# Performance work log

Measured on AMD Instinct MI355X. Metric: run time of the kernel, lower is better.

## Reference

```python
import jax, jax.numpy as jnp
import numpy as np
from math import sqrt

T_TEMP = 1.0  # softmax temperature (init arg T)
NEG_INF = -1e30  # finite stand-in for -inf; masked probs are exactly 0 after softmax


def setup_inputs() -> dict:
    key = jax.random.key(0)
    kq, kk, kv = jax.random.split(key, 3)
    B, L, H, E = 4, 2048, 16, 64
    queries = jax.random.normal(kq, (B, L, H, E), dtype=jnp.float32)
    keys = jax.random.normal(kk, (B, L, H, E), dtype=jnp.float32)
    values = jax.random.normal(kv, (B, L, H, E), dtype=jnp.float32)
    return {"queries": queries, "keys": keys, "values": values}


def reference(queries, keys, values):
    # queries: [B,L,H,E], keys: [B,S,H,E], values: [B,S,H,D]
    B, L, H, E = queries.shape
    S = keys.shape[1]
    scale = 1.0 / sqrt(E)
    # scores: [B,H,L,S]
    scores = jnp.einsum('blhe,bshe->bhls', queries, keys) * scale
    # causal mask: True above diagonal -> masked out (TriangularCausalMask)
    causal = jnp.triu(jnp.ones((L, S), dtype=bool), k=1)
    scores = jnp.where(causal, NEG_INF, scores)
    A = jax.nn.softmax(scores / T_TEMP, axis=-1)  # dropout p=0 -> identity
    V = jnp.einsum('bhls,bshd->blhd', A, values)
    return V
```

## Files before the change

### kernel.cpp

```cpp
#include <hip/hip_runtime.h>


typedef __attribute__((ext_vector_type(8))) unsigned short u16x8;
typedef __attribute__((ext_vector_type(4))) unsigned short u16x4;
typedef __attribute__((ext_vector_type(8))) __bf16 bf16x8;
typedef __attribute__((ext_vector_type(4))) float f32x4;

#define LOG2E 1.44269504088896340736f
#define AS1 __attribute__((address_space(1)))
#define AS3 __attribute__((address_space(3)))

static __device__ __forceinline__ unsigned short f32_bf16_rne(float x) {
    unsigned int b = __builtin_bit_cast(unsigned int, x);
    b = (b + 0x7fffu + ((b >> 16) & 1u)) >> 16;
    return (unsigned short)b;
}

static __device__ __forceinline__ int swzs(int row) {
    return (row & 6) | ((row >> 3) & 1);
}
static __device__ __forceinline__ int tileIdx(int row, int col) {
    return row * 64 + (((col >> 3) ^ swzs(row)) << 3) + (col & 7);
}

__global__ __launch_bounds__(256) void prep_kernel(
    const float* __restrict__ K, const float* __restrict__ V,
    unsigned short* __restrict__ wsK, unsigned short* __restrict__ wsV)
{
    const int ROW = 1024;
    const int tid = threadIdx.x;
    const int kt  = blockIdx.x;
    const int bh  = blockIdx.y;
    const size_t tileBase = (size_t)(bh >> 4) * 2048 * ROW + (size_t)(bh & 15) * 64
                          + (size_t)(kt * 64) * ROW;
    unsigned short* kimg = wsK + (((size_t)bh * 32 + kt) << 12);
    unsigned short* vimg = wsV + (((size_t)bh * 32 + kt) << 12);

    const int kRow = tid >> 4, kCol = (tid & 15) * 4;
    #pragma unroll
    for (int j = 0; j < 4; ++j) {
        const int key = j * 16 + kRow;
        f32x4 v = *(const f32x4*)(K + tileBase + (size_t)key * ROW + kCol);
        u16x4 w;
        #pragma unroll
        for (int i = 0; i < 4; ++i) w[i] = f32_bf16_rne(v[i]);
        *(u16x4*)&kimg[tileIdx(key, kCol)] = w;
    }
    const int vKey2 = (tid & 31) * 2, vDbase = (tid >> 5) * 8;
    const float* r0 = V + tileBase + (size_t)vKey2 * ROW + vDbase;
    #pragma unroll
    for (int j = 0; j < 2; ++j) {
        f32x4 va = *(const f32x4*)(r0 + j * 4);
        f32x4 vb = *(const f32x4*)(r0 + ROW + j * 4);
        #pragma unroll
        for (int i = 0; i < 4; ++i) {
            unsigned int pk = (unsigned int)f32_bf16_rne(va[i])
                            | ((unsigned int)f32_bf16_rne(vb[i]) << 16);
            *(unsigned int*)&vimg[tileIdx(vDbase + j * 4 + i, vKey2)] = pk;
        }
    }
}

__global__ __launch_bounds__(256, 4) void fattn2_kernel(
    const float* __restrict__ Q,
    const unsigned short* __restrict__ wsK,
    const unsigned short* __restrict__ wsV,
    float* __restrict__ O)
{
    const int ROW = 1024;

    const int tid  = threadIdx.x;
    const int wave = tid >> 6;
    const int lane = tid & 63;
    const int quad = lane >> 4;
    const int n16  = lane & 15;

    const int id   = blockIdx.x;
    const int k8   = id & 7;
    const int rest = id >> 3;
    const int bh   = k8 * 8 + (rest >> 4);
    const int xb   = rest & 15;
    const size_t headBase = (size_t)(bh >> 4) * 2048 * ROW + (size_t)(bh & 15) * 64;

    __shared__ __align__(16) unsigned short sK[2][4096];
    __shared__ __align__(16) unsigned short sV[2][4096];
    __shared__ __align__(16) unsigned short sP[4][1024];

    int kvIdx[4];
    #pragma unroll
    for (int nb = 0; nb < 4; ++nb) {
        const int row = nb * 16 + n16;
        kvIdx[nb] = row * 64 + ((quad ^ swzs(row)) << 3);
    }
    const int pIdx = n16 * 64 + ((quad ^ swzs(n16)) << 3);

    const float c0 = 0.125f * LOG2E;

    for (int qi = 0; qi < 2; ++qi) {
        const int qtile = qi ? (31 - xb) : xb;
        const int q0 = qtile * 64 + wave * 16;

        bf16x8 qf0, qf1;
        {
            const float* qrow = Q + headBase + (size_t)(q0 + n16) * ROW + quad * 8;
            u16x8 a, b;
            #pragma unroll
            for (int i = 0; i < 8; ++i) {
                a[i] = f32_bf16_rne(qrow[i] * c0);
                b[i] = f32_bf16_rne(qrow[32 + i] * c0);
            }
            qf0 = __builtin_bit_cast(bf16x8, a);
            qf1 = __builtin_bit_cast(bf16x8, b);
        }

        f32x4 oacc[4];
        #pragma unroll
        for (int d = 0; d < 4; ++d) oacc[d] = (f32x4){0.f, 0.f, 0.f, 0.f};
        float l_r[4];
        #pragma unroll
        for (int r = 0; r < 4; ++r) l_r[r] = 0.f;

        const int nT = qtile + 1;

        #define STAGE(buf, kt_)                                                   \
        do {                                                                      \
            const size_t toff = (((size_t)bh * 32 + (kt_)) << 12);                \
            const unsigned short* kg = wsK + toff + wave * 1024 + lane * 8;       \
            const unsigned short* vg = wsV + toff + wave * 1024 + lane * 8;       \
            __builtin_amdgcn_global_load_lds((const AS1 unsigned int*)kg,         \
                (AS3 unsigned int*)&sK[buf][wave * 1024], 16, 0, 0);              \
            __builtin_amdgcn_global_load_lds((const AS1 unsigned int*)(kg + 512), \
                (AS3 unsigned int*)&sK[buf][wave * 1024 + 512], 16, 0, 0);        \
            __builtin_amdgcn_global_load_lds((const AS1 unsigned int*)vg,         \
                (AS3 unsigned int*)&sV[buf][wave * 1024], 16, 0, 0);              \
            __builtin_amdgcn_global_load_lds((const AS1 unsigned int*)(vg + 512), \
                (AS3 unsigned int*)&sV[buf][wave * 1024 + 512], 16, 0, 0);        \
        } while (0)

        __syncthreads();
        STAGE(0, 0);

        for (int kt = 0; kt < nT; ++kt) {
            const int cur = kt & 1;

            __syncthreads();

            if (kt + 1 < nT) STAGE(cur ^ 1, kt + 1);

            f32x4 sacc[4];
            #pragma unroll
            for (int nb = 0; nb < 4; ++nb) {
                bf16x8 b0 = __builtin_bit_cast(bf16x8, *(const u16x8*)&sK[cur][kvIdx[nb]]);
                bf16x8 b1 = __builtin_bit_cast(bf16x8, *(const u16x8*)&sK[cur][kvIdx[nb] ^ 32]);
                f32x4 s = (f32x4){0.f, 0.f, 0.f, 0.f};
                s = __builtin_amdgcn_mfma_f32_16x16x32_bf16(qf0, b0, s, 0, 0, 0);
                s = __builtin_amdgcn_mfma_f32_16x16x32_bf16(qf1, b1, s, 0, 0, 0);
                sacc[nb] = s;
            }

            if (kt == qtile) {
                #pragma unroll
                for (int nb = 0; nb < 4; ++nb) {
                    const int keyl = nb * 16 + n16;
                    #pragma unroll
                    for (int r = 0; r < 4; ++r) {
                        const int ql = wave * 16 + quad * 4 + r;
                        sacc[nb][r] = (keyl > ql) ? -1e30f : sacc[nb][r];
                    }
                }
            }

            #pragma unroll
            for (int r = 0; r < 4; ++r) {
                const int qrl = quad * 4 + r;
                const int pwBase = qrl * 64 + (n16 & 7);
                const int sw = swzs(qrl);
                const int hb = n16 >> 3;
                float ps = 0.f;
                #pragma unroll
                for (int nb = 0; nb < 4; ++nb) {
                    unsigned short u = f32_bf16_rne(__builtin_amdgcn_exp2f(sacc[nb][r]));
                    ps += __builtin_bit_cast(float, (unsigned int)u << 16);
                    sP[wave][pwBase + (((nb * 2 + hb) ^ sw) << 3)] = u;
                }
                l_r[r] += ps;
            }

            #pragma unroll
            for (int kh = 0; kh < 2; ++kh) {
                bf16x8 ap = __builtin_bit_cast(bf16x8,
                    *(const u16x8*)&sP[wave][pIdx ^ (kh << 5)]);
                #pragma unroll
                for (int d = 0; d < 4; ++d) {
                    bf16x8 vf = __builtin_bit_cast(bf16x8,
                        *(const u16x8*)&sV[cur][kvIdx[d] ^ (kh << 5)]);
                    oacc[d] = __builtin_amdgcn_mfma_f32_16x16x32_bf16(ap, vf, oacc[d], 0, 0, 0);
                }
            }
        }
        #undef STAGE

        float inv[4];
        #pragma unroll
        for (int r = 0; r < 4; ++r) {
            float l = l_r[r];
            #pragma unroll
            for (int off = 1; off < 16; off <<= 1)
                l += __shfl_xor(l, off, 64);
            inv[r] = 1.0f / l;
        }
        #pragma unroll
        for (int d = 0; d < 4; ++d) {
            #pragma unroll
            for (int r = 0; r < 4; ++r) {
                const int qg = q0 + quad * 4 + r;
                O[headBase + (size_t)qg * ROW + d * 16 + n16] = oacc[d][r] * inv[r];
            }
        }
    }
}

__global__ __launch_bounds__(256, 4) void fattn_kernel(
    const float* __restrict__ Q,
    const float* __restrict__ K,
    const float* __restrict__ V,
    float* __restrict__ O)
{
    const int ROW = 1024;
    const int tid  = threadIdx.x;
    const int wave = tid >> 6;
    const int lane = tid & 63;
    const int quad = lane >> 4;
    const int n16  = lane & 15;
    const int xb = blockIdx.x;
    const int bh = blockIdx.y;
    const size_t headBase = (size_t)(bh >> 4) * 2048 * ROW + (size_t)(bh & 15) * 64;

    __shared__ __align__(16) unsigned short sK[4096];
    __shared__ __align__(16) unsigned short sV[4096];
    __shared__ __align__(16) unsigned short sP[4][1024];

    int kvIdx[4];
    #pragma unroll
    for (int nb = 0; nb < 4; ++nb) {
        const int row = nb * 16 + n16;
        kvIdx[nb] = row * 64 + ((quad ^ swzs(row)) << 3);
    }
    const int pIdx = n16 * 64 + ((quad ^ swzs(n16)) << 3);
    const int kStageRow = tid >> 4;
    const int kStageCol = (tid & 15) * 4;
    const int vKey2  = (tid & 31) * 2;
    const int vDbase = (tid >> 5) * 8;
    const float c0 = 0.125f * LOG2E;

    for (int qi = 0; qi < 2; ++qi) {
        const int qtile = qi ? (31 - xb) : xb;
        const int q0 = qtile * 64 + wave * 16;
        bf16x8 qf0, qf1;
        {
            const float* qrow = Q + headBase + (size_t)(q0 + n16) * ROW + quad * 8;
            u16x8 a, b;
            #pragma unroll
            for (int i = 0; i < 8; ++i) {
                a[i] = f32_bf16_rne(qrow[i] * c0);
                b[i] = f32_bf16_rne(qrow[32 + i] * c0);
            }
            qf0 = __builtin_bit_cast(bf16x8, a);
            qf1 = __builtin_bit_cast(bf16x8, b);
        }
        f32x4 oacc[4];
        #pragma unroll
        for (int d = 0; d < 4; ++d) oacc[d] = (f32x4){0.f, 0.f, 0.f, 0.f};
        float l_r[4];
        #pragma unroll
        for (int r = 0; r < 4; ++r) l_r[r] = 0.f;
        const int nT = qtile + 1;
        f32x4 pk[4], pva[2], pvb[2];
        {
            const float* kb = K + headBase;
            const float* r0 = V + headBase + (size_t)vKey2 * ROW + vDbase;
            #pragma unroll
            for (int j = 0; j < 4; ++j)
                pk[j] = *(const f32x4*)(kb + (size_t)(j * 16 + kStageRow) * ROW + kStageCol);
            #pragma unroll
            for (int j = 0; j < 2; ++j) {
                pva[j] = *(const f32x4*)(r0 + j * 4);
                pvb[j] = *(const f32x4*)(r0 + ROW + j * 4);
            }
        }
        for (int kt = 0; kt < nT; ++kt) {
            __syncthreads();
            #pragma unroll
            for (int j = 0; j < 4; ++j) {
                u16x4 w;
                #pragma unroll
                for (int i = 0; i < 4; ++i) w[i] = f32_bf16_rne(pk[j][i]);
                *(u16x4*)&sK[tileIdx(j * 16 + kStageRow, kStageCol)] = w;
            }
            #pragma unroll
            for (int j = 0; j < 2; ++j) {
                const int d0 = vDbase + j * 4;
                #pragma unroll
                for (int i = 0; i < 4; ++i) {
                    unsigned int pkk = (unsigned int)f32_bf16_rne(pva[j][i])
                                     | ((unsigned int)f32_bf16_rne(pvb[j][i]) << 16);
                    *(unsigned int*)&sV[tileIdx(d0 + i, vKey2)] = pkk;
                }
            }
            if (kt + 1 < nT) {
                const size_t nb2 = headBase + (size_t)((kt + 1) * 64) * ROW;
                const float* kb = K + nb2;
                const float* r0 = V + nb2 + (size_t)vKey2 * ROW + vDbase;
                #pragma unroll
                for (int j = 0; j < 4; ++j)
                    pk[j] = *(const f32x4*)(kb + (size_t)(j * 16 + kStageRow) * ROW + kStageCol);
                #pragma unroll
                for (int j = 0; j < 2; ++j) {
                    pva[j] = *(const f32x4*)(r0 + j * 4);
                    pvb[j] = *(const f32x4*)(r0 + ROW + j * 4);
                }
            }
            __syncthreads();
            f32x4 sacc[4];
            #pragma unroll
            for (int nb = 0; nb < 4; ++nb) {
                bf16x8 b0 = __builtin_bit_cast(bf16x8, *(const u16x8*)&sK[kvIdx[nb]]);
                bf16x8 b1 = __builtin_bit_cast(bf16x8, *(const u16x8*)&sK[kvIdx[nb] ^ 32]);
                f32x4 s = (f32x4){0.f, 0.f, 0.f, 0.f};
                s = __builtin_amdgcn_mfma_f32_16x16x32_bf16(qf0, b0, s, 0, 0, 0);
                s = __builtin_amdgcn_mfma_f32_16x16x32_bf16(qf1, b1, s, 0, 0, 0);
                sacc[nb] = s;
            }
            if (kt == qtile) {
                #pragma unroll
                for (int nb = 0; nb < 4; ++nb) {
                    const int keyl = nb * 16 + n16;
                    #pragma unroll
                    for (int r = 0; r < 4; ++r) {
                        const int ql = wave * 16 + quad * 4 + r;
                        sacc[nb][r] = (keyl > ql) ? -1e30f : sacc[nb][r];
                    }
                }
            }
            #pragma unroll
            for (int r = 0; r < 4; ++r) {
                const int qrl = quad * 4 + r;
                const int pwBase = qrl * 64 + (n16 & 7);
                const int sw = swzs(qrl);
                const int hb = n16 >> 3;
                float ps = 0.f;
                #pragma unroll
                for (int nb = 0; nb < 4; ++nb) {
                    unsigned short u = f32_bf16_rne(__builtin_amdgcn_exp2f(sacc[nb][r]));
                    ps += __builtin_bit_cast(float, (unsigned int)u << 16);
                    sP[wave][pwBase + (((nb * 2 + hb) ^ sw) << 3)] = u;
                }
                l_r[r] += ps;
            }
            #pragma unroll
            for (int kh = 0; kh < 2; ++kh) {
                bf16x8 ap = __builtin_bit_cast(bf16x8,
                    *(const u16x8*)&sP[wave][pIdx ^ (kh << 5)]);
                #pragma unroll
                for (int d = 0; d < 4; ++d) {
                    bf16x8 vf = __builtin_bit_cast(bf16x8,
                        *(const u16x8*)&sV[kvIdx[d] ^ (kh << 5)]);
                    oacc[d] = __builtin_amdgcn_mfma_f32_16x16x32_bf16(ap, vf, oacc[d], 0, 0, 0);
                }
            }
        }
        float inv[4];
        #pragma unroll
        for (int r = 0; r < 4; ++r) {
            float l = l_r[r];
            #pragma unroll
            for (int off = 1; off < 16; off <<= 1)
                l += __shfl_xor(l, off, 64);
            inv[r] = 1.0f / l;
        }
        #pragma unroll
        for (int d = 0; d < 4; ++d) {
            #pragma unroll
            for (int r = 0; r < 4; ++r) {
                const int qg = q0 + quad * 4 + r;
                O[headBase + (size_t)qg * ROW + d * 16 + n16] = oacc[d][r] * inv[r];
            }
        }
    }
}

extern "C" void kernel_launch(void* const* d_in, const int* in_sizes, int n_in,
                              void* d_out, int out_size, void* d_ws, size_t ws_size,
                              hipStream_t stream) {
    const float* Q = (const float*)d_in[0];
    const float* K = (const float*)d_in[1];
    const float* V = (const float*)d_in[2];
    float* Out = (float*)d_out;

    const size_t imgElems = (size_t)64 * 32 * 4096;
    if (ws_size >= imgElems * 2 * sizeof(unsigned short)) {
        unsigned short* wsK = (unsigned short*)d_ws;
        unsigned short* wsV = wsK + imgElems;
        hipLaunchKernelGGL(prep_kernel, dim3(32, 64), dim3(256), 0, stream, K, V, wsK, wsV);
        hipLaunchKernelGGL(fattn2_kernel, dim3(1024), dim3(256), 0, stream, Q, wsK, wsV, Out);
    } else {
        hipLaunchKernelGGL(fattn_kernel, dim3(16, 64), dim3(256), 0, stream, Q, K, V, Out);
    }
}
```

Baseline: 200.1 us.

## Keep softmax probabilities in registers, transpose MFMA, one q-tile per block

The attention kernel now computes S^T by swapping MFMA operands, so each lane holds probabilities for a single query row. P is rearranged into B-operand layout with cross-lane shuffles instead of a round trip through shared memory, which removes the sP buffer. Each block now handles one q-tile, longest first, over 2048 blocks with launch bounds raised to 5 blocks per CU. Output is transposed through LDS for coalesced f32x4 stores, and conversions use packed v_cvt_pk_bf16_f32. The prep kernel transposes V through padded LDS so global writes are vectorized. The cost is extra shuffles, register pressure from the higher occupancy target, and less even load balance across blocks.

```diff
diff --git a/kernel.cpp b/kernel.cpp
--- a/kernel.cpp
+++ b/kernel.cpp
@@ -5,6 +5,7 @@
 typedef __attribute__((ext_vector_type(4))) unsigned short u16x4;
 typedef __attribute__((ext_vector_type(8))) __bf16 bf16x8;
 typedef __attribute__((ext_vector_type(4))) float f32x4;
+typedef __attribute__((ext_vector_type(4))) unsigned int u32x4;
 
 #define LOG2E 1.44269504088896340736f
 #define AS1 __attribute__((address_space(1)))
@@ -14,6 +15,12 @@
     unsigned int b = __builtin_bit_cast(unsigned int, x);
     b = (b + 0x7fffu + ((b >> 16) & 1u)) >> 16;
     return (unsigned short)b;
+}
+
+static __device__ __forceinline__ unsigned int cvt_pk_bf16(float lo, float hi) {
+    unsigned int r;
+    asm("v_cvt_pk_bf16_f32 %0, %1, %2" : "=v"(r) : "v"(lo), "v"(hi));
+    return r;
 }
 
 static __device__ __forceinline__ int swzs(int row) {
@@ -36,6 +43,8 @@
     unsigned short* kimg = wsK + (((size_t)bh * 32 + kt) << 12);
     unsigned short* vimg = wsV + (((size_t)bh * 32 + kt) << 12);
 
+    __shared__ unsigned int sT[64 * 33];
+
     const int kRow = tid >> 4, kCol = (tid & 15) * 4;
     #pragma unroll
     for (int j = 0; j < 4; ++j) {
@@ -46,22 +55,33 @@
         for (int i = 0; i < 4; ++i) w[i] = f32_bf16_rne(v[i]);
         *(u16x4*)&kimg[tileIdx(key, kCol)] = w;
     }
-    const int vKey2 = (tid & 31) * 2, vDbase = (tid >> 5) * 8;
-    const float* r0 = V + tileBase + (size_t)vKey2 * ROW + vDbase;
-    #pragma unroll
-    for (int j = 0; j < 2; ++j) {
-        f32x4 va = *(const f32x4*)(r0 + j * 4);
-        f32x4 vb = *(const f32x4*)(r0 + ROW + j * 4);
-        #pragma unroll
-        for (int i = 0; i < 4; ++i) {
-            unsigned int pk = (unsigned int)f32_bf16_rne(va[i])
-                            | ((unsigned int)f32_bf16_rne(vb[i]) << 16);
-            *(unsigned int*)&vimg[tileIdx(vDbase + j * 4 + i, vKey2)] = pk;
-        }
-    }
-}
-
-__global__ __launch_bounds__(256, 4) void fattn2_kernel(
+
+    const int rp = tid >> 3;
+    const int cc = tid & 7;
+    const float* v0 = V + tileBase + (size_t)(2 * rp) * ROW + cc * 8;
+    f32x4 a0 = *(const f32x4*)(v0);
+    f32x4 a1 = *(const f32x4*)(v0 + 4);
+    f32x4 b0 = *(const f32x4*)(v0 + ROW);
+    f32x4 b1 = *(const f32x4*)(v0 + ROW + 4);
+    #pragma unroll
+    for (int i = 0; i < 4; ++i) {
+        sT[(cc * 8 + i) * 33 + rp]     = cvt_pk_bf16(a0[i], b0[i]);
+        sT[(cc * 8 + 4 + i) * 33 + rp] = cvt_pk_bf16(a1[i], b1[i]);
+    }
+    __syncthreads();
+    const int d = tid >> 2;
+    #pragma unroll
+    for (int it = 0; it < 2; ++it) {
+        const int p = (tid & 3) + it * 4;
+        const int c = p ^ swzs(d);
+        u32x4 w;
+        #pragma unroll
+        for (int j = 0; j < 4; ++j) w[j] = sT[d * 33 + c * 4 + j];
+        *(u32x4*)&vimg[(size_t)d * 64 + p * 8] = w;
+    }
+}
+
+__global__ __launch_bounds__(256, 5) void fattn2_kernel(
     const float* __restrict__ Q,
     const unsigned short* __restrict__ wsK,
     const unsigned short* __restrict__ wsV,
@@ -74,17 +94,19 @@
     const int lane = tid & 63;
     const int quad = lane >> 4;
     const int n16  = lane & 15;
-
-    const int id   = blockIdx.x;
-    const int k8   = id & 7;
-    const int rest = id >> 3;
-    const int bh   = k8 * 8 + (rest >> 4);
-    const int xb   = rest & 15;
+    const bool hi16 = (lane & 16) != 0;
+    const bool hi32 = (lane & 32) != 0;
+
+    const int id    = blockIdx.x;
+    const int k8    = id & 7;
+    const int rest  = id >> 3;
+    const int bh    = k8 * 8 + (rest >> 5);
+    const int qtile = 31 - (rest & 31);
     const size_t headBase = (size_t)(bh >> 4) * 2048 * ROW + (size_t)(bh & 15) * 64;
+    const int q0 = qtile * 64 + wave * 16;
 
     __shared__ __align__(16) unsigned short sK[2][4096];
     __shared__ __align__(16) unsigned short sV[2][4096];
-    __shared__ __align__(16) unsigned short sP[4][1024];
 
     int kvIdx[4];
     #pragma unroll
@@ -92,131 +114,153 @@
         const int row = nb * 16 + n16;
         kvIdx[nb] = row * 64 + ((quad ^ swzs(row)) << 3);
     }
-    const int pIdx = n16 * 64 + ((quad ^ swzs(n16)) << 3);
 
     const float c0 = 0.125f * LOG2E;
 
-    for (int qi = 0; qi < 2; ++qi) {
-        const int qtile = qi ? (31 - xb) : xb;
-        const int q0 = qtile * 64 + wave * 16;
-
-        bf16x8 qf0, qf1;
-        {
-            const float* qrow = Q + headBase + (size_t)(q0 + n16) * ROW + quad * 8;
-            u16x8 a, b;
-            #pragma unroll
-            for (int i = 0; i < 8; ++i) {
-                a[i] = f32_bf16_rne(qrow[i] * c0);
-                b[i] = f32_bf16_rne(qrow[32 + i] * c0);
-            }
-            qf0 = __builtin_bit_cast(bf16x8, a);
-            qf1 = __builtin_bit_cast(bf16x8, b);
-        }
-
-        f32x4 oacc[4];
-        #pragma unroll
-        for (int d = 0; d < 4; ++d) oacc[d] = (f32x4){0.f, 0.f, 0.f, 0.f};
-        float l_r[4];
-        #pragma unroll
-        for (int r = 0; r < 4; ++r) l_r[r] = 0.f;
-
-        const int nT = qtile + 1;
-
-        #define STAGE(buf, kt_)                                                   \
-        do {                                                                      \
-            const size_t toff = (((size_t)bh * 32 + (kt_)) << 12);                \
-            const unsigned short* kg = wsK + toff + wave * 1024 + lane * 8;       \
-            const unsigned short* vg = wsV + toff + wave * 1024 + lane * 8;       \
-            __builtin_amdgcn_global_load_lds((const AS1 unsigned int*)kg,         \
-                (AS3 unsigned int*)&sK[buf][wave * 1024], 16, 0, 0);              \
-            __builtin_amdgcn_global_load_lds((const AS1 unsigned int*)(kg + 512), \
-                (AS3 unsigned int*)&sK[buf][wave * 1024 + 512], 16, 0, 0);        \
-            __builtin_amdgcn_global_load_lds((const AS1 unsigned int*)vg,         \
-                (AS3 unsigned int*)&sV[buf][wave * 1024], 16, 0, 0);              \
-            __builtin_amdgcn_global_load_lds((const AS1 unsigned int*)(vg + 512), \
-                (AS3 unsigned int*)&sV[buf][wave * 1024 + 512], 16, 0, 0);        \
-        } while (0)
+    bf16x8 qf0, qf1;
+    {
+        const float* qrow = Q + headBase + (size_t)(q0 + n16) * ROW + quad * 8;
+        f32x4 qv0 = *(const f32x4*)(qrow);
+        f32x4 qv1 = *(const f32x4*)(qrow + 4);
+        f32x4 qv2 = *(const f32x4*)(qrow + 32);
+        f32x4 qv3 = *(const f32x4*)(qrow + 36);
+        u32x4 a, b;
+        a[0] = cvt_pk_bf16(qv0[0] * c0, qv0[1] * c0);
+        a[1] = cvt_pk_bf16(qv0[2] * c0, qv0[3] * c0);
+        a[2] = cvt_pk_bf16(qv1[0] * c0, qv1[1] * c0);
+        a[3] = cvt_pk_bf16(qv1[2] * c0, qv1[3] * c0);
+        b[0] = cvt_pk_bf16(qv2[0] * c0, qv2[1] * c0);
+        b[1] = cvt_pk_bf16(qv2[2] * c0, qv2[3] * c0);
+        b[2] = cvt_pk_bf16(qv3[0] * c0, qv3[1] * c0);
+        b[3] = cvt_pk_bf16(qv3[2] * c0, qv3[3] * c0);
+        qf0 = __builtin_bit_cast(bf16x8, a);
+        qf1 = __builtin_bit_cast(bf16x8, b);
+    }
+
+    f32x4 oacc[4];
+    #pragma unroll
+    for (int dd = 0; dd < 4; ++dd) oacc[dd] = (f32x4){0.f, 0.f, 0.f, 0.f};
+    float l = 0.f;
+
+    const int nT = qtile + 1;
+
+    #define STAGE(buf, kt_)                                                   \
+    do {                                                                      \
+        const size_t toff = (((size_t)bh * 32 + (kt_)) << 12);                \
+        const unsigned short* kg = wsK + toff + wave * 1024 + lane * 8;       \
+        const unsigned short* vg = wsV + toff + wave * 1024 + lane * 8;       \
+        __builtin_amdgcn_global_load_lds((const AS1 unsigned int*)kg,         \
+            (AS3 unsigned int*)&sK[buf][wave * 1024], 16, 0, 0);              \
+        __builtin_amdgcn_global_load_lds((const AS1 unsigned int*)(kg + 512), \
+            (AS3 unsigned int*)&sK[buf][wave * 1024 + 512], 16, 0, 0);        \
+        __builtin_amdgcn_global_load_lds((const AS1 unsigned int*)vg,         \
+            (AS3 unsigned int*)&sV[buf][wave * 1024], 16, 0, 0);              \
+        __builtin_amdgcn_global_load_lds((const AS1 unsigned int*)(vg + 512), \
+            (AS3 unsigned int*)&sV[buf][wave * 1024 + 512], 16, 0, 0);        \
+    } while (0)
+
+    STAGE(0, 0);
+
+    for (int kt = 0; kt < nT; ++kt) {
+        const int cur = kt & 1;
 
         __syncthreads();
-        STAGE(0, 0);
-
-        for (int kt = 0; kt < nT; ++kt) {
-            const int cur = kt & 1;
-
-            __syncthreads();
-
-            if (kt + 1 < nT) STAGE(cur ^ 1, kt + 1);
-
-            f32x4 sacc[4];
+
+        if (kt + 1 < nT) STAGE(cur ^ 1, kt + 1);
+
+        f32x4 sacc[4];
+        #pragma unroll
+        for (int nb = 0; nb < 4; ++nb) {
+            bf16x8 b0 = __builtin_bit_cast(bf16x8, *(const u16x8*)&sK[cur][kvIdx[nb]]);
+            bf16x8 b1 = __builtin_bit_cast(bf16x8, *(const u16x8*)&sK[cur][kvIdx[nb] ^ 32]);
+            f32x4 s = (f32x4){0.f, 0.f, 0.f, 0.f};
+            s = __builtin_amdgcn_mfma_f32_16x16x32_bf16(b0, qf0, s, 0, 0, 0);
+            s = __builtin_amdgcn_mfma_f32_16x16x32_bf16(b1, qf1, s, 0, 0, 0);
+            sacc[nb] = s;
+        }
+
+        if (kt == qtile) {
+            const int ql = wave * 16 + n16;
             #pragma unroll
             for (int nb = 0; nb < 4; ++nb) {
-                bf16x8 b0 = __builtin_bit_cast(bf16x8, *(const u16x8*)&sK[cur][kvIdx[nb]]);
-                bf16x8 b1 = __builtin_bit_cast(bf16x8, *(const u16x8*)&sK[cur][kvIdx[nb] ^ 32]);
-                f32x4 s = (f32x4){0.f, 0.f, 0.f, 0.f};
-                s = __builtin_amdgcn_mfma_f32_16x16x32_bf16(qf0, b0, s, 0, 0, 0);
-                s = __builtin_amdgcn_mfma_f32_16x16x32_bf16(qf1, b1, s, 0, 0, 0);
-                sacc[nb] = s;
-            }
-
-            if (kt == qtile) {
-                #pragma unroll
-                for (int nb = 0; nb < 4; ++nb) {
-                    const int keyl = nb * 16 + n16;
-                    #pragma unroll
-                    for (int r = 0; r < 4; ++r) {
-                        const int ql = wave * 16 + quad * 4 + r;
-                        sacc[nb][r] = (keyl > ql) ? -1e30f : sacc[nb][r];
-                    }
-                }
-            }
-
-            #pragma unroll
-            for (int r = 0; r < 4; ++r) {
-                const int qrl = quad * 4 + r;
-                const int pwBase = qrl * 64 + (n16 & 7);
-                const int sw = swzs(qrl);
-                const int hb = n16 >> 3;
-                float ps = 0.f;
-                #pragma unroll
-                for (int nb = 0; nb < 4; ++nb) {
-                    unsigned short u = f32_bf16_rne(__builtin_amdgcn_exp2f(sacc[nb][r]));
-                    ps += __builtin_bit_cast(float, (unsigned int)u << 16);
-                    sP[wave][pwBase + (((nb * 2 + hb) ^ sw) << 3)] = u;
-                }
-                l_r[r] += ps;
-            }
-
-            #pragma unroll
-            for (int kh = 0; kh < 2; ++kh) {
-                bf16x8 ap = __builtin_bit_cast(bf16x8,
-                    *(const u16x8*)&sP[wave][pIdx ^ (kh << 5)]);
-                #pragma unroll
-                for (int d = 0; d < 4; ++d) {
-                    bf16x8 vf = __builtin_bit_cast(bf16x8,
-                        *(const u16x8*)&sV[cur][kvIdx[d] ^ (kh << 5)]);
-                    oacc[d] = __builtin_amdgcn_mfma_f32_16x16x32_bf16(ap, vf, oacc[d], 0, 0, 0);
-                }
-            }
-        }
-        #undef STAGE
-
-        float inv[4];
-        #pragma unroll
-        for (int r = 0; r < 4; ++r) {
-            float l = l_r[r];
-            #pragma unroll
-            for (int off = 1; off < 16; off <<= 1)
-                l += __shfl_xor(l, off, 64);
-            inv[r] = 1.0f / l;
-        }
-        #pragma unroll
-        for (int d = 0; d < 4; ++d) {
-            #pragma unroll
-            for (int r = 0; r < 4; ++r) {
-                const int qg = q0 + quad * 4 + r;
-                O[headBase + (size_t)qg * ROW + d * 16 + n16] = oacc[d][r] * inv[r];
-            }
-        }
+                #pragma unroll
+                for (int r = 0; r < 4; ++r) {
+                    const int keyl = nb * 16 + quad * 4 + r;
+                    sacc[nb][r] = (keyl > ql) ? -1e30f : sacc[nb][r];
+                }
+            }
+        }
+
+        unsigned int W[4][2];
+        float psum = 0.f;
+        #pragma unroll
+        for (int nb = 0; nb < 4; ++nb) {
+            float p0 = __builtin_amdgcn_exp2f(sacc[nb][0]);
+            float p1 = __builtin_amdgcn_exp2f(sacc[nb][1]);
+            float p2 = __builtin_amdgcn_exp2f(sacc[nb][2]);
+            float p3 = __builtin_amdgcn_exp2f(sacc[nb][3]);
+            psum += (p0 + p1) + (p2 + p3);
+            W[nb][0] = cvt_pk_bf16(p0, p1);
+            W[nb][1] = cvt_pk_bf16(p2, p3);
+        }
+        l += psum;
+
+        #pragma unroll
+        for (int kh = 0; kh < 2; ++kh) {
+            const unsigned int A0 = W[2 * kh][0],     A1 = W[2 * kh][1];
+            const unsigned int B0 = W[2 * kh + 1][0], B1 = W[2 * kh + 1][1];
+            const unsigned int sA0 = __shfl_xor(A0, 32, 64);
+            const unsigned int sB0 = __shfl_xor(B0, 32, 64);
+            const unsigned int sA1 = __shfl_xor(A1, 32, 64);
+            const unsigned int sB1 = __shfl_xor(B1, 32, 64);
+            const unsigned int X0p0 = hi32 ? sB0 : A0;
+            const unsigned int X1p0 = hi32 ? B0 : sA0;
+            const unsigned int X0p1 = hi32 ? sB1 : A1;
+            const unsigned int X1p1 = hi32 ? B1 : sA1;
+            const unsigned int t0 = __shfl_xor(X1p0, 16, 64);
+            const unsigned int t1 = __shfl_xor(X0p0, 16, 64);
+            const unsigned int t2 = __shfl_xor(X1p1, 16, 64);
+            const unsigned int t3 = __shfl_xor(X0p1, 16, 64);
+            u32x4 bw;
+            bw[0] = hi16 ? t0 : X0p0;
+            bw[1] = hi16 ? t2 : X0p1;
+            bw[2] = hi16 ? X1p0 : t1;
+            bw[3] = hi16 ? X1p1 : t3;
+            const bf16x8 bp = __builtin_bit_cast(bf16x8, bw);
+            #pragma unroll
+            for (int dd = 0; dd < 4; ++dd) {
+                bf16x8 vf = __builtin_bit_cast(bf16x8,
+                    *(const u16x8*)&sV[cur][kvIdx[dd] ^ (kh << 5)]);
+                oacc[dd] = __builtin_amdgcn_mfma_f32_16x16x32_bf16(vf, bp, oacc[dd], 0, 0, 0);
+            }
+        }
+    }
+    #undef STAGE
+
+    float lt = l;
+    lt += __shfl_xor(lt, 16, 64);
+    lt += __shfl_xor(lt, 32, 64);
+    const float inv = 1.0f / lt;
+    #pragma unroll
+    for (int dd = 0; dd < 4; ++dd)
+        #pragma unroll
+        for (int r = 0; r < 4; ++r) oacc[dd][r] *= inv;
+
+    __syncthreads();
+    float* tb = (float*)&sK[0][0] + wave * 1024;
+    #pragma unroll
+    for (int dd = 0; dd < 4; ++dd) {
+        const int slot = ((dd * 4) | quad) ^ n16;
+        *(f32x4*)&tb[n16 * 64 + slot * 4] = oacc[dd];
+    }
+    const int rrow  = lane >> 2;
+    const int cbase = lane & 3;
+    #pragma unroll
+    for (int it = 0; it < 4; ++it) {
+        const int cc   = cbase + it * 4;
+        const int slot = cc ^ rrow;
+        f32x4 v = *(const f32x4*)&tb[rrow * 64 + slot * 4];
+        *(f32x4*)&O[headBase + (size_t)(q0 + rrow) * ROW + cc * 4] = v;
     }
 }
 
@@ -402,7 +446,7 @@
         unsigned short* wsK = (unsigned short*)d_ws;
         unsigned short* wsV = wsK + imgElems;
         hipLaunchKernelGGL(prep_kernel, dim3(32, 64), dim3(256), 0, stream, K, V, wsK, wsV);
-        hipLaunchKernelGGL(fattn2_kernel, dim3(1024), dim3(256), 0, stream, Q, wsK, wsV, Out);
+        hipLaunchKernelGGL(fattn2_kernel, dim3(2048), dim3(256), 0, stream, Q, wsK, wsV, Out);
     } else {
         hipLaunchKernelGGL(fattn_kernel, dim3(16, 64), dim3(256), 0, stream, Q, K, V, Out);
     }
```

After: 213.3 us. 1.07x slower.
